# Kernel optimization log

Measured on AMD Instinct MI355X. Metric: run time of the kernel, lower is better.

Reference implementation:

```python
import jax, jax.numpy as jnp
import numpy as np
from jax import lax

E = 256
H = 8
DH = E // H


def _layernorm(x, g, b, eps=1e-5):
    mu = jnp.mean(x, axis=-1, keepdims=True)
    var = jnp.var(x, axis=-1, keepdims=True)
    return (x - mu) * lax.rsqrt(var + eps) * g + b


def _mha(x, Wqkv, bqkv, Wo, bo):
    B, S, _ = x.shape
    qkv = x @ Wqkv.T + bqkv                     # [B,S,3E]
    q, k, v = jnp.split(qkv, 3, axis=-1)
    def heads(t):
        return t.reshape(B, S, H, DH).transpose(0, 2, 1, 3)  # [B,H,S,DH]
    q, k, v = heads(q), heads(k), heads(v)
    scores = jnp.einsum('bhqd,bhkd->bhqk', q, k) / jnp.sqrt(jnp.float32(DH)).astype(x.dtype)
    attn = jax.nn.softmax(scores, axis=-1)
    ctx = jnp.einsum('bhqk,bhkd->bhqd', attn, v)
    ctx = ctx.transpose(0, 2, 1, 3).reshape(B, S, E)
    return ctx @ Wo.T + bo


def _encoder_layer(x, p):
    g1, b1, Wqkv, bqkv, Wo, bo, g2, b2, W1, bf1, W2, bf2 = p
    # norm_first pre-LN block (dropout=0)
    x = x + _mha(_layernorm(x, g1, b1), Wqkv, bqkv, Wo, bo)
    h = _layernorm(x, g2, b2)
    h = jax.nn.gelu(h @ W1.T + bf1, approximate=False) @ W2.T + bf2
    return x + h


def setup_inputs() -> dict:
    key = jax.random.key(0)
    ks = jax.random.split(key, 20)
    B, S, L = 16, 1024, 2
    s = 0.02
    inp = {
        'text_embeddings': jax.random.normal(ks[0], (B, S, 768), jnp.float32),
        'image_embeddings': jax.random.normal(ks[1], (B, S, 2048), jnp.float32),
        'text_mask': jnp.ones((B, S), jnp.float32),
        'image_mask': jnp.ones((B, S), jnp.float32),
        'pos_emb': jax.random.normal(ks[2], (1, S, E), jnp.float32) * s,
        'text_W': jax.random.normal(ks[3], (E, 768), jnp.float32) * s,
        'text_b': jnp.zeros((E,), jnp.float32),
        'img_W': jax.random.normal(ks[4], (E, 2048), jnp.float32) * s,
        'img_b': jnp.zeros((E,), jnp.float32),
        'ln1_g': jnp.ones((L, E), jnp.float32),
        'ln1_b': jnp.zeros((L, E), jnp.float32),
        'qkv_W': jax.random.normal(ks[5], (L, 3 * E, E), jnp.float32) * s,
        'qkv_b': jnp.zeros((L, 3 * E), jnp.float32),
        'out_W': jax.random.normal(ks[6], (L, E, E), jnp.float32) * s,
        'out_b': jnp.zeros((L, E), jnp.float32),
        'ln2_g': jnp.ones((L, E), jnp.float32),
        'ln2_b': jnp.zeros((L, E), jnp.float32),
        'ffn_W1': jax.random.normal(ks[7], (L, 4 * E, E), jnp.float32) * s,
        'ffn_b1': jnp.zeros((L, 4 * E), jnp.float32),
        'ffn_W2': jax.random.normal(ks[8], (L, E, 4 * E), jnp.float32) * s,
        'ffn_b2': jnp.zeros((L, E), jnp.float32),
        'cls_W': jax.random.normal(ks[9], (1, E), jnp.float32) * s,
        'cls_b': jnp.zeros((1,), jnp.float32),
        'i2h_W': jax.random.normal(ks[10], (E, 2 * E), jnp.float32) * s,
        'i2h_b': jnp.zeros((E,), jnp.float32),
        'h2o_W': jax.random.normal(ks[11], (E, E), jnp.float32) * s,
        'h2o_b': jnp.zeros((E,), jnp.float32),
        'h0': jax.random.uniform(ks[12], (B, E), jnp.float32),
    }
    return inp


def reference(text_embeddings, image_embeddings, text_mask, image_mask, pos_emb,
              text_W, text_b, img_W, img_b,
              ln1_g, ln1_b, qkv_W, qkv_b, out_W, out_b, ln2_g, ln2_b,
              ffn_W1, ffn_b1, ffn_W2, ffn_b2,
              cls_W, cls_b, i2h_W, i2h_b, h2o_W, h2o_b, h0):
    lang = text_embeddings @ text_W.T + text_b + pos_emb   # [B,S,E]
    visn = image_embeddings @ img_W.T + img_b + pos_emb    # computed, unused (0 cross layers)
    x = lang
    L = qkv_W.shape[0]
    for l in range(L):
        x = _encoder_layer(x, (ln1_g[l], ln1_b[l], qkv_W[l], qkv_b[l], out_W[l], out_b[l],
                               ln2_g[l], ln2_b[l], ffn_W1[l], ffn_b1[l], ffn_W2[l], ffn_b2[l]))
    final_vector = x                                       # [B,S,E]

    def step(h, x_t):
        combined = jnp.concatenate([x_t, h], axis=1)       # [B,2E]
        h = jnp.tanh(combined @ i2h_W.T + i2h_b)
        h = h * (h > 0.0).astype(h.dtype)                  # threshold mask
        out = h @ h2o_W.T + h2o_b
        return h, out

    _, outs = lax.scan(step, h0, final_vector.transpose(1, 0, 2))  # outs: [S,B,E]
    ssm = outs[-1]
    logits = ssm @ cls_W.T + cls_b                         # [B,1]
    probas = jax.nn.sigmoid(logits)
    return logits, probas, final_vector, ssm
```

## Files before the change

### kernel.cpp

```cpp
#include <hip/hip_runtime.h>
#include <hip/hip_bf16.h>
#include <math.h>

typedef __bf16 bf16_t;
typedef __bf16 bf16x8 __attribute__((ext_vector_type(8)));
typedef __bf16 bf16x4 __attribute__((ext_vector_type(4)));
typedef float  f32x4  __attribute__((ext_vector_type(4)));

#define DEVI static __device__ __forceinline__

DEVI f32x4 mfma16(bf16x8 a, bf16x8 b, f32x4 c) {
    return __builtin_amdgcn_mfma_f32_16x16x32_bf16(a, b, c, 0, 0, 0);
}

__global__ void cast4_k(const float* __restrict__ src, bf16_t* __restrict__ dst, int n4) {
    int i = blockIdx.x * 256 + threadIdx.x;
    if (i < n4) {
        float4 v = ((const float4*)src)[i];
        bf16x4 o;
        o[0] = (bf16_t)v.x; o[1] = (bf16_t)v.y; o[2] = (bf16_t)v.z; o[3] = (bf16_t)v.w;
        *(bf16x4*)(dst + (long)i * 4) = o;
    }
}

__global__ __launch_bounds__(256) void ln_k(const float* __restrict__ x,
                                            const float* __restrict__ g,
                                            const float* __restrict__ bta,
                                            bf16_t* __restrict__ out) {
    int wave = threadIdx.x >> 6, lane = threadIdx.x & 63;
    int row = blockIdx.x * 4 + wave;
    const float4 v = *(const float4*)(x + (long)row * 256 + lane * 4);
    float s  = v.x + v.y + v.z + v.w;
    float s2 = v.x * v.x + v.y * v.y + v.z * v.z + v.w * v.w;
    for (int m = 1; m < 64; m <<= 1) { s += __shfl_xor(s, m); s2 += __shfl_xor(s2, m); }
    float mu  = s * (1.f / 256.f);
    float var = s2 * (1.f / 256.f) - mu * mu;
    float rs  = rsqrtf(var + 1e-5f);
    float4 gg = *(const float4*)(g + lane * 4);
    float4 bb = *(const float4*)(bta + lane * 4);
    bf16x4 o;
    o[0] = (bf16_t)((v.x - mu) * rs * gg.x + bb.x);
    o[1] = (bf16_t)((v.y - mu) * rs * gg.y + bb.y);
    o[2] = (bf16_t)((v.z - mu) * rs * gg.z + bb.z);
    o[3] = (bf16_t)((v.w - mu) * rs * gg.w + bb.w);
    *(bf16x4*)(out + (long)row * 256 + lane * 4) = o;
}

enum { EPI_PROJ = 0, EPI_QKV = 1, EPI_RESID = 2, EPI_GELU = 3, EPI_XPROJ = 4 };

template <int EPI>
__global__ __launch_bounds__(256) void gemm_bt(
    const bf16_t* __restrict__ A, int lda,
    const bf16_t* __restrict__ W, int ldw,
    const float* __restrict__ bias,
    int N, int K,
    bf16_t* __restrict__ outb, int ldob,
    float* __restrict__ outf,
    const float* __restrict__ pos,
    bf16_t* __restrict__ vt) {
    int tiles_n = N >> 6;
    int tm = blockIdx.x / tiles_n, tn = blockIdx.x % tiles_n;
    int wave = threadIdx.x >> 6, lane = threadIdx.x & 63;
    int quad = lane >> 4, l16 = lane & 15;
    int m0 = tm * 64 + wave * 16;
    int n0 = tn * 64;
    const bf16_t* a_ptr = A + (long)(m0 + l16) * lda + quad * 8;
    const bf16_t* w_ptr = W + (long)(n0 + l16) * ldw + quad * 8;
    f32x4 zero = {0.f, 0.f, 0.f, 0.f};
    f32x4 acc[4] = {zero, zero, zero, zero};
    for (int k = 0; k < K; k += 32) {
        bf16x8 af = *(const bf16x8*)(a_ptr + k);
#pragma unroll
        for (int c = 0; c < 4; ++c) {
            bf16x8 wf = *(const bf16x8*)(w_ptr + (long)c * 16 * ldw + k);
            acc[c] = mfma16(af, wf, acc[c]);
        }
    }
#pragma unroll
    for (int c = 0; c < 4; ++c) {
        int col = n0 + c * 16 + l16;
        float bv = bias[col];
#pragma unroll
        for (int r = 0; r < 4; ++r) {
            int row = m0 + quad * 4 + r;
            float v = acc[c][r] + bv;
            if (EPI == EPI_PROJ) {
                int s = row & 1023;
                v += pos[(long)s * 256 + col];
                outf[(long)row * 256 + col] = v;
            } else if (EPI == EPI_QKV) {
                outb[(long)row * ldob + col] = (bf16_t)v;
                if (col >= 512) {
                    int b = row >> 10, s = row & 1023;
                    int hh = (col - 512) >> 5, d = (col - 512) & 31;
                    vt[(((long)(b * 8 + hh) * 32 + d) << 10) + s] = (bf16_t)v;
                }
            } else if (EPI == EPI_RESID) {
                float* p = outf + (long)row * 256 + col;
                *p = *p + v;
            } else if (EPI == EPI_GELU) {
                float gg = 0.5f * v * (1.f + erff(v * 0.70710678118654752f));
                outb[(long)row * ldob + col] = (bf16_t)gg;
            } else if (EPI == EPI_XPROJ) {
                int b = row >> 10, s = row & 1023;
                outb[((long)(s * 256 + col)) * 16 + b] = (bf16_t)v;
            }
        }
    }
}

__global__ __launch_bounds__(256) void attn_k(const bf16_t* __restrict__ qkv,
                                              const bf16_t* __restrict__ vt,
                                              bf16_t* __restrict__ ctx) {
    __shared__ bf16_t Pbuf[4][16 * 32];
    int wave = threadIdx.x >> 6, lane = threadIdx.x & 63;
    int quad = lane >> 4, l16 = lane & 15;
    int bh = blockIdx.x >> 4;
    int b = bh >> 3, h = bh & 7;
    int q0 = ((blockIdx.x & 15) * 4 + wave) * 16;
    const bf16_t* qbase = qkv + (long)(b * 1024 + q0 + l16) * 768 + h * 32 + quad * 8;
    bf16x8 qf = *(const bf16x8*)qbase;
    const bf16_t* kbase = qkv + (long)(b * 1024 + l16) * 768 + 256 + h * 32 + quad * 8;
    const bf16_t* vbase = vt + ((long)bh * 32) * 1024;
    f32x4 zero = {0.f, 0.f, 0.f, 0.f};
    f32x4 ca = zero, cb = zero;
    float mrow[4] = {-INFINITY, -INFINITY, -INFINITY, -INFINITY};
    float lrow[4] = {0.f, 0.f, 0.f, 0.f};
    bf16_t* P = Pbuf[wave];
    const float sc = 0.17677669529663687f;
    for (int kb = 0; kb < 1024; kb += 32) {
        bf16x8 kf0 = *(const bf16x8*)(kbase + (long)kb * 768);
        bf16x8 kf1 = *(const bf16x8*)(kbase + (long)(kb + 16) * 768);
        f32x4 s0 = mfma16(qf, kf0, zero);
        f32x4 s1 = mfma16(qf, kf1, zero);
        float p0[4], p1[4];
#pragma unroll
        for (int r = 0; r < 4; ++r) {
            float a0 = s0[r] * sc, a1 = s1[r] * sc;
            float mx = fmaxf(a0, a1);
            mx = fmaxf(mx, __shfl_xor(mx, 1));
            mx = fmaxf(mx, __shfl_xor(mx, 2));
            mx = fmaxf(mx, __shfl_xor(mx, 4));
            mx = fmaxf(mx, __shfl_xor(mx, 8));
            float mn = fmaxf(mrow[r], mx);
            float alpha = __expf(mrow[r] - mn);
            mrow[r] = mn;
            float e0 = __expf(a0 - mn), e1 = __expf(a1 - mn);
            float rs = e0 + e1;
            rs += __shfl_xor(rs, 1);
            rs += __shfl_xor(rs, 2);
            rs += __shfl_xor(rs, 4);
            rs += __shfl_xor(rs, 8);
            lrow[r] = lrow[r] * alpha + rs;
            ca[r] *= alpha;
            cb[r] *= alpha;
            p0[r] = e0; p1[r] = e1;
        }
#pragma unroll
        for (int r = 0; r < 4; ++r) {
            P[(quad * 4 + r) * 32 + l16] = (bf16_t)p0[r];
            P[(quad * 4 + r) * 32 + 16 + l16] = (bf16_t)p1[r];
        }
        __syncthreads();
        bf16x8 pf = *(const bf16x8*)(P + l16 * 32 + quad * 8);
        bf16x8 vf0 = *(const bf16x8*)(vbase + (long)l16 * 1024 + kb + quad * 8);
        bf16x8 vf1 = *(const bf16x8*)(vbase + (long)(16 + l16) * 1024 + kb + quad * 8);
        ca = mfma16(pf, vf0, ca);
        cb = mfma16(pf, vf1, cb);
        __syncthreads();
    }
#pragma unroll
    for (int r = 0; r < 4; ++r) {
        float inv = 1.f / lrow[r];
        long row = (long)(b * 1024 + q0 + quad * 4 + r);
        ctx[row * 256 + h * 32 + l16] = (bf16_t)(ca[r] * inv);
        ctx[row * 256 + h * 32 + 16 + l16] = (bf16_t)(cb[r] * inv);
    }
}

__global__ __launch_bounds__(256, 1) void scan_k(const bf16_t* __restrict__ xpb,
                                                 const bf16_t* __restrict__ wi2h,
                                                 const bf16_t* __restrict__ wh2o,
                                                 const float* __restrict__ h2o_b,
                                                 const float* __restrict__ cls_W,
                                                 const float* __restrict__ cls_b,
                                                 const float* __restrict__ h0,
                                                 float* __restrict__ d_out) {
    constexpr int HS = 264;
    __shared__ bf16_t hbuf[2][16 * HS];
    __shared__ float ssm_lds[16 * 256];
    int tid = threadIdx.x;
    int w = tid >> 6, lane = tid & 63, quad = lane >> 4, l16 = lane & 15;
    bf16x8 whf[4][8];
#pragma unroll
    for (int c = 0; c < 4; ++c) {
        const bf16_t* p = wi2h + (long)(w * 64 + c * 16 + l16) * 512 + 256 + quad * 8;
#pragma unroll
        for (int ks = 0; ks < 8; ++ks) whf[c][ks] = *(const bf16x8*)(p + ks * 32);
    }
    {
        int b = tid >> 4, e0 = (tid & 15) * 16;
        const float4* src = (const float4*)(h0 + b * 256 + e0);
        bf16_t* dst = &hbuf[0][b * HS + e0];
#pragma unroll
        for (int j = 0; j < 4; ++j) {
            float4 v = src[j];
            bf16x4 o;
            o[0] = (bf16_t)v.x; o[1] = (bf16_t)v.y; o[2] = (bf16_t)v.z; o[3] = (bf16_t)v.w;
            *(bf16x4*)(dst + j * 4) = o;
        }
    }
    __syncthreads();
    f32x4 zero = {0.f, 0.f, 0.f, 0.f};
    bf16x4 xcur[4], xnxt[4];
#pragma unroll
    for (int c = 0; c < 4; ++c)
        xcur[c] = *(const bf16x4*)(xpb + ((long)(w * 64 + c * 16 + l16) * 16 + quad * 4));
    for (int t = 0; t < 1024; ++t) {
        int tn = (t + 1) & 1023;
#pragma unroll
        for (int c = 0; c < 4; ++c)
            xnxt[c] = *(const bf16x4*)(xpb + ((long)(tn * 256 + w * 64 + c * 16 + l16) * 16 + quad * 4));
        const bf16_t* hb = hbuf[t & 1];
        f32x4 acc[4] = {zero, zero, zero, zero};
#pragma unroll
        for (int ks = 0; ks < 8; ++ks) {
            bf16x8 af = *(const bf16x8*)(hb + l16 * HS + ks * 32 + quad * 8);
#pragma unroll
            for (int c = 0; c < 4; ++c) acc[c] = mfma16(af, whf[c][ks], acc[c]);
        }
        bf16_t* hn = hbuf[(t + 1) & 1];
#pragma unroll
        for (int c = 0; c < 4; ++c) {
#pragma unroll
            for (int r = 0; r < 4; ++r) {
                float u = acc[c][r] + (float)xcur[c][r];
                float ex = __expf(-2.f * u);
                float th = (1.f - ex) * __builtin_amdgcn_rcpf(1.f + ex);
                th = (u > 0.f) ? th : 0.f;
                hn[(quad * 4 + r) * HS + w * 64 + c * 16 + l16] = (bf16_t)th;
            }
            xcur[c] = xnxt[c];
        }
        __syncthreads();
    }
    const bf16_t* hf = hbuf[0];
    float* ssm_out = d_out + 32 + 4194304;
#pragma unroll
    for (int c = 0; c < 4; ++c) {
        int e = w * 64 + c * 16 + l16;
        const bf16_t* p = wh2o + (long)e * 256 + quad * 8;
        f32x4 a = zero;
#pragma unroll
        for (int ks = 0; ks < 8; ++ks) {
            bf16x8 af = *(const bf16x8*)(hf + l16 * HS + ks * 32 + quad * 8);
            a = mfma16(af, *(const bf16x8*)(p + ks * 32), a);
        }
        float bv = h2o_b[e];
#pragma unroll
        for (int r = 0; r < 4; ++r) {
            int b = quad * 4 + r;
            float v = a[r] + bv;
            ssm_out[(long)b * 256 + e] = v;
            ssm_lds[b * 256 + e] = v;
        }
    }
    __syncthreads();
    {
        int b = tid >> 4, sub = tid & 15;
        float s = 0.f;
#pragma unroll
        for (int j = 0; j < 16; ++j) s += ssm_lds[b * 256 + sub * 16 + j] * cls_W[sub * 16 + j];
        s += __shfl_xor(s, 1);
        s += __shfl_xor(s, 2);
        s += __shfl_xor(s, 4);
        s += __shfl_xor(s, 8);
        if (sub == 0) {
            float lg = s + cls_b[0];
            d_out[b] = lg;
            d_out[16 + b] = 1.f / (1.f + __expf(-lg));
        }
    }
}

extern "C" void kernel_launch(void* const* d_in, const int* in_sizes, int n_in,
                              void* d_out, int out_size, void* d_ws, size_t ws_size,
                              hipStream_t stream) {
    const float* text_emb = (const float*)d_in[0];
    const float* pos_emb  = (const float*)d_in[4];
    const float* text_W   = (const float*)d_in[5];
    const float* text_b   = (const float*)d_in[6];
    const float* ln1_g    = (const float*)d_in[9];
    const float* ln1_b    = (const float*)d_in[10];
    const float* qkv_W    = (const float*)d_in[11];
    const float* qkv_b    = (const float*)d_in[12];
    const float* out_W    = (const float*)d_in[13];
    const float* out_b    = (const float*)d_in[14];
    const float* ln2_g    = (const float*)d_in[15];
    const float* ln2_b    = (const float*)d_in[16];
    const float* ffn_W1   = (const float*)d_in[17];
    const float* ffn_b1   = (const float*)d_in[18];
    const float* ffn_W2   = (const float*)d_in[19];
    const float* ffn_b2   = (const float*)d_in[20];
    const float* cls_W    = (const float*)d_in[21];
    const float* cls_b    = (const float*)d_in[22];
    const float* i2h_W    = (const float*)d_in[23];
    const float* i2h_b    = (const float*)d_in[24];
    const float* h2o_W    = (const float*)d_in[25];
    const float* h2o_b    = (const float*)d_in[26];
    const float* h0       = (const float*)d_in[27];

    char* ws = (char*)d_ws;
    bf16_t* wtext = (bf16_t*)(ws + 0);
    bf16_t* wqkv  = (bf16_t*)(ws + 393216);
    bf16_t* wout  = (bf16_t*)(ws + 1179648);
    bf16_t* wff1  = (bf16_t*)(ws + 1441792);
    bf16_t* wff2  = (bf16_t*)(ws + 2490368);
    bf16_t* wi2h  = (bf16_t*)(ws + 3538944);
    bf16_t* wh2o  = (bf16_t*)(ws + 3801088);
    bf16_t* buf1  = (bf16_t*)(ws + 4194304);
    bf16_t* buf2  = (bf16_t*)(ws + 37748736);
    bf16_t* buf3  = (bf16_t*)(ws + 62914560);
    bf16_t* buf4  = (bf16_t*)(ws + 71303168);
    bf16_t* buf5  = (bf16_t*)(ws + 79691776);
    bf16_t* xpb   = (bf16_t*)(ws + 37748736);
    float*  xbuf  = (float*)d_out + 32;

    auto cast = [&](const float* s, bf16_t* d, long n) {
        cast4_k<<<(int)((n / 4 + 255) / 256), 256, 0, stream>>>(s, d, (int)(n / 4));
    };
    cast(text_W, wtext, 196608);
    cast(qkv_W, wqkv, 393216);
    cast(out_W, wout, 131072);
    cast(ffn_W1, wff1, 524288);
    cast(ffn_W2, wff2, 524288);
    cast(i2h_W, wi2h, 131072);
    cast(h2o_W, wh2o, 65536);
    cast(text_emb, buf1, (long)16384 * 768);

    gemm_bt<EPI_PROJ><<<256 * 4, 256, 0, stream>>>(buf1, 768, wtext, 768, text_b, 256, 768,
                                                   nullptr, 0, xbuf, pos_emb, nullptr);
    for (int l = 0; l < 2; ++l) {
        ln_k<<<4096, 256, 0, stream>>>(xbuf, ln1_g + l * 256, ln1_b + l * 256, buf3);
        gemm_bt<EPI_QKV><<<256 * 12, 256, 0, stream>>>(buf3, 256, wqkv + l * 196608, 256,
                                                       qkv_b + l * 768, 768, 256,
                                                       buf2, 768, nullptr, nullptr, buf5);
        attn_k<<<2048, 256, 0, stream>>>(buf2, buf5, buf4);
        gemm_bt<EPI_RESID><<<256 * 4, 256, 0, stream>>>(buf4, 256, wout + l * 65536, 256,
                                                        out_b + l * 256, 256, 256,
                                                        nullptr, 0, xbuf, nullptr, nullptr);
        ln_k<<<4096, 256, 0, stream>>>(xbuf, ln2_g + l * 256, ln2_b + l * 256, buf3);
        gemm_bt<EPI_GELU><<<256 * 16, 256, 0, stream>>>(buf3, 256, wff1 + l * 262144, 256,
                                                        ffn_b1 + l * 1024, 1024, 256,
                                                        buf1, 1024, nullptr, nullptr, nullptr);
        gemm_bt<EPI_RESID><<<256 * 4, 256, 0, stream>>>(buf1, 1024, wff2 + l * 262144, 1024,
                                                        ffn_b2 + l * 256, 256, 1024,
                                                        nullptr, 0, xbuf, nullptr, nullptr);
    }
    cast(xbuf, buf3, (long)16384 * 256);
    gemm_bt<EPI_XPROJ><<<256 * 4, 256, 0, stream>>>(buf3, 256, wi2h, 512, i2h_b, 256, 256,
                                                    xpb, 0, nullptr, nullptr, nullptr);
    scan_k<<<1, 256, 0, stream>>>(xpb, wi2h, wh2o, h2o_b, cls_W, cls_b, h0, (float*)d_out);
}
```

Before: 2.059 ms.

## Transpose scan MFMA operands, seed accumulators with fp32 input projection, split K chains

The serial RNN scan now swaps the MFMA operand order so each lane owns four consecutive hidden units. Each lane can then write the new hidden state to LDS as one bf16x4 vector store instead of four scalar stores. The input projection is stored in fp32 in [s,b,e] layout and loaded straight into the accumulators, which removes a separate add and the bf16 rounding of that input. The K loop is split into two independent accumulator chains to shorten the MFMA dependency latency in the 1024-step critical path, and the threshold is simplified to a max with zero. The cost is twice the memory traffic for the projection buffer and more registers.

```diff
diff --git a/kernel.cpp b/kernel.cpp
--- a/kernel.cpp
+++ b/kernel.cpp
@@ -103,7 +103,7 @@
                 outb[(long)row * ldob + col] = (bf16_t)gg;
             } else if (EPI == EPI_XPROJ) {
                 int b = row >> 10, s = row & 1023;
-                outb[((long)(s * 256 + col)) * 16 + b] = (bf16_t)v;
+                outf[((long)(s * 16 + b)) * 256 + col] = v;
             }
         }
     }
@@ -178,7 +178,7 @@
     }
 }
 
-__global__ __launch_bounds__(256, 1) void scan_k(const bf16_t* __restrict__ xpb,
+__global__ __launch_bounds__(256, 1) void scan_k(const float* __restrict__ xp,
                                                  const bf16_t* __restrict__ wi2h,
                                                  const bf16_t* __restrict__ wh2o,
                                                  const float* __restrict__ h2o_b,
@@ -212,34 +212,46 @@
     }
     __syncthreads();
     f32x4 zero = {0.f, 0.f, 0.f, 0.f};
-    bf16x4 xcur[4], xnxt[4];
-#pragma unroll
-    for (int c = 0; c < 4; ++c)
-        xcur[c] = *(const bf16x4*)(xpb + ((long)(w * 64 + c * 16 + l16) * 16 + quad * 4));
+    const long xoff = (long)l16 * 256 + w * 64 + quad * 4;
+    f32x4 xcur[4], xnxt[4];
+#pragma unroll
+    for (int c = 0; c < 4; ++c) xcur[c] = *(const f32x4*)(xp + xoff + c * 16);
     for (int t = 0; t < 1024; ++t) {
         int tn = (t + 1) & 1023;
-#pragma unroll
-        for (int c = 0; c < 4; ++c)
-            xnxt[c] = *(const bf16x4*)(xpb + ((long)(tn * 256 + w * 64 + c * 16 + l16) * 16 + quad * 4));
+        const float* xb_n = xp + (long)tn * 4096 + xoff;
+#pragma unroll
+        for (int c = 0; c < 4; ++c) xnxt[c] = *(const f32x4*)(xb_n + c * 16);
         const bf16_t* hb = hbuf[t & 1];
-        f32x4 acc[4] = {zero, zero, zero, zero};
-#pragma unroll
-        for (int ks = 0; ks < 8; ++ks) {
-            bf16x8 af = *(const bf16x8*)(hb + l16 * HS + ks * 32 + quad * 8);
-#pragma unroll
-            for (int c = 0; c < 4; ++c) acc[c] = mfma16(af, whf[c][ks], acc[c]);
-        }
+        f32x4 accL[4], accH[4];
+#pragma unroll
+        for (int c = 0; c < 4; ++c) { accL[c] = xcur[c]; accH[c] = zero; }
+        bf16x8 hfrag[4];
+#pragma unroll
+        for (int ks = 0; ks < 4; ++ks)
+            hfrag[ks] = *(const bf16x8*)(hb + l16 * HS + ks * 32 + quad * 8);
+#pragma unroll
+        for (int ks = 0; ks < 4; ++ks)
+#pragma unroll
+            for (int c = 0; c < 4; ++c) accL[c] = mfma16(whf[c][ks], hfrag[ks], accL[c]);
+#pragma unroll
+        for (int ks = 0; ks < 4; ++ks)
+            hfrag[ks] = *(const bf16x8*)(hb + l16 * HS + (ks + 4) * 32 + quad * 8);
+#pragma unroll
+        for (int ks = 0; ks < 4; ++ks)
+#pragma unroll
+            for (int c = 0; c < 4; ++c) accH[c] = mfma16(whf[c][ks + 4], hfrag[ks], accH[c]);
         bf16_t* hn = hbuf[(t + 1) & 1];
 #pragma unroll
         for (int c = 0; c < 4; ++c) {
+            f32x4 u4 = accL[c] + accH[c];
+            bf16x4 o;
 #pragma unroll
             for (int r = 0; r < 4; ++r) {
-                float u = acc[c][r] + (float)xcur[c][r];
-                float ex = __expf(-2.f * u);
+                float ex = fminf(__expf(-2.f * u4[r]), 1e37f);
                 float th = (1.f - ex) * __builtin_amdgcn_rcpf(1.f + ex);
-                th = (u > 0.f) ? th : 0.f;
-                hn[(quad * 4 + r) * HS + w * 64 + c * 16 + l16] = (bf16_t)th;
+                o[r] = (bf16_t)fmaxf(th, 0.f);
             }
+            *(bf16x4*)(hn + l16 * HS + w * 64 + c * 16 + quad * 4) = o;
             xcur[c] = xnxt[c];
         }
         __syncthreads();
@@ -248,22 +260,17 @@
     float* ssm_out = d_out + 32 + 4194304;
 #pragma unroll
     for (int c = 0; c < 4; ++c) {
-        int e = w * 64 + c * 16 + l16;
-        const bf16_t* p = wh2o + (long)e * 256 + quad * 8;
+        const bf16_t* p = wh2o + (long)(w * 64 + c * 16 + l16) * 256 + quad * 8;
         f32x4 a = zero;
 #pragma unroll
         for (int ks = 0; ks < 8; ++ks) {
             bf16x8 af = *(const bf16x8*)(hf + l16 * HS + ks * 32 + quad * 8);
-            a = mfma16(af, *(const bf16x8*)(p + ks * 32), a);
-        }
-        float bv = h2o_b[e];
-#pragma unroll
-        for (int r = 0; r < 4; ++r) {
-            int b = quad * 4 + r;
-            float v = a[r] + bv;
-            ssm_out[(long)b * 256 + e] = v;
-            ssm_lds[b * 256 + e] = v;
-        }
+            a = mfma16(*(const bf16x8*)(p + ks * 32), af, a);
+        }
+        float4 bv = *(const float4*)(h2o_b + w * 64 + c * 16 + quad * 4);
+        float4 v = {a[0] + bv.x, a[1] + bv.y, a[2] + bv.z, a[3] + bv.w};
+        *(float4*)(ssm_out + (long)l16 * 256 + w * 64 + c * 16 + quad * 4) = v;
+        *(float4*)(&ssm_lds[l16 * 256 + w * 64 + c * 16 + quad * 4]) = v;
     }
     __syncthreads();
     {
@@ -323,7 +330,7 @@
     bf16_t* buf3  = (bf16_t*)(ws + 62914560);
     bf16_t* buf4  = (bf16_t*)(ws + 71303168);
     bf16_t* buf5  = (bf16_t*)(ws + 79691776);
-    bf16_t* xpb   = (bf16_t*)(ws + 37748736);
+    float*  xp    = (float*)(ws + 37748736);
     float*  xbuf  = (float*)d_out + 32;
 
     auto cast = [&](const float* s, bf16_t* d, long n) {
@@ -359,6 +366,6 @@
     }
     cast(xbuf, buf3, (long)16384 * 256);
     gemm_bt<EPI_XPROJ><<<256 * 4, 256, 0, stream>>>(buf3, 256, wi2h, 512, i2h_b, 256, 256,
-                                                    xpb, 0, nullptr, nullptr, nullptr);
-    scan_k<<<1, 256, 0, stream>>>(xpb, wi2h, wh2o, h2o_b, cls_W, cls_b, h0, (float*)d_out);
-}
+                                                    nullptr, 0, xp, nullptr, nullptr);
+    scan_k<<<1, 256, 0, stream>>>(xp, wi2h, wh2o, h2o_b, cls_W, cls_b, h0, (float*)d_out);
+}
```

Result: slower. 2.575 ms (+25.1%).
